# Performance work log

Measured on AMD Instinct MI355X. Metric: run time of the kernel, lower is better.

The kernel has to match this reference:

```python
import jax, jax.numpy as jnp
import numpy as np

E = 8      # number of experts (sublayers)
N = 8192   # tokens / batch rows
D = 1024   # sublayer input size (max_sublayer_input_size)
H = 2048   # sublayer output size
O = 1024   # output_encoding_size


def setup_inputs() -> dict:
    key = jax.random.key(0)
    k0, k1, k2, k3 = jax.random.split(key, 4)
    x_feat = jax.random.normal(k0, (N, D), dtype=jnp.float32)
    expert_idx = jax.random.randint(k1, (N,), 0, E)  # exclusive (top-1) routing
    # Stacked expert params: sublayers = Linear(D,H), encoders = Linear(H,O)
    W1 = jax.random.normal(k2, (E, D, H), dtype=jnp.float32) * (1.0 / np.sqrt(D))
    b1 = jnp.zeros((E, H), dtype=jnp.float32)
    W2 = jax.random.normal(k3, (E, H, O), dtype=jnp.float32) * (1.0 / np.sqrt(H))
    b2 = jnp.zeros((E, O), dtype=jnp.float32)
    return {"x_feat": x_feat, "W1": W1, "b1": b1, "W2": W2, "b2": b2,
            "expert_idx": expert_idx}


def reference(x_feat, W1, b1, W2, b2, expert_idx):
    # one-hot sublayer_mask (last E columns of the original x)
    onehot = jax.nn.one_hot(expert_idx, E, dtype=x_feat.dtype)  # [N, E]
    # Exclusive dispatch: each token goes through exactly one expert.
    # Structural loop over the fixed E experts; combine via the one-hot mask
    # (equivalent to the original gather -> sublayer -> encoder -> scatter).
    enc = jnp.zeros((x_feat.shape[0], O), dtype=x_feat.dtype)
    for i in range(E):
        h = x_feat @ W1[i] + b1[i]          # [N, H] sublayer
        y = h @ W2[i] + b2[i]               # [N, O] encoder
        enc = enc + onehot[:, i:i + 1] * y  # keep only rows routed to expert i
    # output = [encoded (O cols) | sublayer_mask (E cols)]
    return jnp.concatenate([enc, onehot], axis=1)
```

## Files before the change

### kernel.cpp

```cpp
#include <hip/hip_runtime.h>

#define NTOK 8192
#define DDIM 1024
#define HDIM 2048
#define ODIM 1024
#define NEXP 8
#define OUTW (ODIM + NEXP)
#define MT_MAX 64

typedef __bf16 bf16_t;
typedef bf16_t bf16x8 __attribute__((ext_vector_type(8)));
typedef bf16_t bf16x4 __attribute__((ext_vector_type(4)));
typedef float f32x4 __attribute__((ext_vector_type(4)));

__device__ __forceinline__ void gld_lds16(bf16_t* lds, const bf16_t* g) {
  __builtin_amdgcn_global_load_lds(
      (__attribute__((address_space(1))) void*)g,
      (__attribute__((address_space(3))) void*)lds, 16, 0, 0);
}

__global__ void zero_cnt_kernel(int* cnt) {
  if (threadIdx.x < NEXP) cnt[threadIdx.x] = 0;
}

__global__ void route_kernel(const int* __restrict__ idx, float* __restrict__ out,
                             int* __restrict__ rank, int* cnt) {
  __shared__ int lcnt[NEXP];
  __shared__ int lbase[NEXP];
  int t = threadIdx.x;
  if (t < NEXP) lcnt[t] = 0;
  __syncthreads();
  int n = blockIdx.x * 256 + t;
  int e = idx[n];
  int lr = atomicAdd(&lcnt[e], 1);
  __syncthreads();
  if (t < NEXP) lbase[t] = atomicAdd(&cnt[t], lcnt[t]);
  __syncthreads();
  rank[n] = lbase[e] + lr;
  float* o = out + (size_t)n * OUTW + ODIM;
#pragma unroll
  for (int j = 0; j < NEXP; j++) o[j] = (j == e) ? 1.0f : 0.0f;
}

__global__ void scan_kernel(const int* __restrict__ cnt, int* __restrict__ off) {
  if (threadIdx.x == 0) {
    int s = 0;
    for (int e = 0; e < NEXP; e++) { off[e] = s; s += cnt[e]; }
  }
}

__global__ void gather_kernel(const float* __restrict__ x, const int* __restrict__ idx,
                              const int* __restrict__ rank, const int* __restrict__ off,
                              bf16_t* __restrict__ xg, int* __restrict__ tok_of_pos) {
  int n = blockIdx.x;
  int e = idx[n];
  int pos = off[e] + rank[n];
  if (threadIdx.x == 0) tok_of_pos[pos] = n;
  float4 v = ((const float4*)(x + (size_t)n * DDIM))[threadIdx.x];
  bf16x4 o;
  o[0] = (bf16_t)v.x; o[1] = (bf16_t)v.y; o[2] = (bf16_t)v.z; o[3] = (bf16_t)v.w;
  *(bf16x4*)(xg + (size_t)pos * DDIM + threadIdx.x * 4) = o;
}

__global__ __launch_bounds__(256) void wtrans_kernel(const float* __restrict__ src,
                                                     bf16_t* __restrict__ dst,
                                                     int R, int C) {
  __shared__ float t[128][65];
  int e = blockIdx.z;
  int c0 = blockIdx.x * 64, r0g = blockIdx.y * 128;
  int tid = threadIdx.x;
  const float* s = src + (size_t)e * R * C;
#pragma unroll
  for (int p = 0; p < 8; p++) {
    int r = (tid >> 4) + p * 16;
    int c4 = (tid & 15) * 4;
    float4 v = *(const float4*)&s[(size_t)(r0g + r) * C + c0 + c4];
    t[r][c4 + 0] = v.x;
    t[r][c4 + 1] = v.y;
    t[r][c4 + 2] = v.z;
    t[r][c4 + 3] = v.w;
  }
  __syncthreads();
  bf16_t* d = dst + (size_t)e * R * C;
  int w = tid >> 6, l = tid & 63;
#pragma unroll
  for (int itc = 0; itc < 2; itc++) {
#pragma unroll
    for (int it2 = 0; it2 < 2; it2++) {
      int c = (l >> 3) + 8 * w + 32 * itc;
      int r0 = (l & 7) * 8 + 64 * it2;
      bf16x8 o;
#pragma unroll
      for (int j = 0; j < 8; j++) o[j] = (bf16_t)t[r0 + j][c];
      *(bf16x8*)&d[(size_t)(c0 + c) * R + r0g + r0] = o;
    }
  }
}

template <int KDIM, int NCOLS, int MTG, bool TO_BF16>
__global__ __launch_bounds__(256) void gemm_kernel(
    const bf16_t* __restrict__ A, const bf16_t* __restrict__ Bt,
    const float* __restrict__ bias,
    const int* __restrict__ cnt, const int* __restrict__ off,
    const int* __restrict__ tok_of_pos,
    bf16_t* __restrict__ outb, float* __restrict__ outf) {
  constexpr int NT = NCOLS / 128;
  const int b = blockIdx.x;
  const int e = b & 7;
  int t = b >> 3;
  const int mtl = t % MTG;
  t /= MTG;
  const int nt = t % NT;
  const int g = t / NT;
  const int mt = g * MTG + mtl;

  const int count = cnt[e];
  if (mt * 128 >= count) return;
  const int base = off[e];

  __shared__ bf16_t lA[128 * 32];
  __shared__ bf16_t lB[128 * 32];

  const int tid = threadIdx.x;
  const int lane = tid & 63;
  const int wave = tid >> 6;
  const int mrow = lane & 15;
  const int q = lane >> 4;
  const int wm = (wave & 1) * 64;
  const int wn = (wave >> 1) * 64;

  const bf16_t* pA[2];
  const bf16_t* pB[2];
#pragma unroll
  for (int s = 0; s < 2; s++) {
    int lrow = wave * 32 + s * 16 + (lane >> 2);
    int kq = (lane & 3) ^ (lrow & 3);
    int gr = base + mt * 128 + lrow;
    if (gr > NTOK - 1) gr = NTOK - 1;
    pA[s] = A + (size_t)gr * KDIM + kq * 8;
    int nrow = nt * 128 + lrow;
    pB[s] = Bt + ((size_t)e * NCOLS + nrow) * KDIM + kq * 8;
  }

  f32x4 acc[4][4] = {};
  const bf16_t* la0 = &lA[(wm + mrow) * 32 + ((q ^ (mrow & 3)) * 8)];
  const bf16_t* lb0 = &lB[(wn + mrow) * 32 + ((q ^ (mrow & 3)) * 8)];

  for (int kk = 0; kk < KDIM; kk += 32) {
#pragma unroll
    for (int s = 0; s < 2; s++) {
      gld_lds16(&lA[(wave * 2 + s) * 512], pA[s] + kk);
      gld_lds16(&lB[(wave * 2 + s) * 512], pB[s] + kk);
    }
    __syncthreads();
    bf16x8 af[4], bfr[4];
#pragma unroll
    for (int i = 0; i < 4; i++) {
      af[i]  = *(const bf16x8*)(la0 + i * 16 * 32);
      bfr[i] = *(const bf16x8*)(lb0 + i * 16 * 32);
    }
#pragma unroll
    for (int i = 0; i < 4; i++)
#pragma unroll
      for (int j = 0; j < 4; j++)
        acc[i][j] = __builtin_amdgcn_mfma_f32_16x16x32_bf16(af[i], bfr[j], acc[i][j], 0, 0, 0);
    __syncthreads();
  }

  const int mlimit = count - mt * 128;
  float bs[4];
#pragma unroll
  for (int j = 0; j < 4; j++)
    bs[j] = bias[(size_t)e * NCOLS + nt * 128 + wn + j * 16 + mrow];

#pragma unroll
  for (int i = 0; i < 4; i++) {
#pragma unroll
    for (int r = 0; r < 4; r++) {
      int ml = wm + i * 16 + q * 4 + r;
      if (ml < mlimit) {
        int prow = base + mt * 128 + ml;
        if constexpr (TO_BF16) {
          bf16_t* orow = outb + (size_t)prow * NCOLS;
#pragma unroll
          for (int j = 0; j < 4; j++)
            orow[nt * 128 + wn + j * 16 + mrow] = (bf16_t)(acc[i][j][r] + bs[j]);
        } else {
          int tok = tok_of_pos[prow];
          float* orow = outf + (size_t)tok * OUTW;
#pragma unroll
          for (int j = 0; j < 4; j++)
            orow[nt * 128 + wn + j * 16 + mrow] = acc[i][j][r] + bs[j];
        }
      }
    }
  }
}

extern "C" void kernel_launch(void* const* d_in, const int* in_sizes, int n_in,
                              void* d_out, int out_size, void* d_ws, size_t ws_size,
                              hipStream_t stream) {
  const float* x  = (const float*)d_in[0];
  const float* W1 = (const float*)d_in[1];
  const float* b1 = (const float*)d_in[2];
  const float* W2 = (const float*)d_in[3];
  const float* b2 = (const float*)d_in[4];
  const int* idx  = (const int*)d_in[5];
  float* out = (float*)d_out;

  char* ws = (char*)d_ws;
  bf16_t* xg  = (bf16_t*)(ws);
  bf16_t* hg  = (bf16_t*)(ws + 16777216);
  bf16_t* Wt1 = (bf16_t*)(ws + 50331648);
  bf16_t* Wt2 = (bf16_t*)(ws + 83886080);
  int* tok    = (int*)(ws + 117440512);
  int* rank   = (int*)(ws + 117473280);
  int* cnt    = (int*)(ws + 117506048);
  int* off    = (int*)(ws + 117506080);

  zero_cnt_kernel<<<1, 64, 0, stream>>>(cnt);
  route_kernel<<<NTOK / 256, 256, 0, stream>>>(idx, out, rank, cnt);
  scan_kernel<<<1, 64, 0, stream>>>(cnt, off);
  gather_kernel<<<NTOK, 256, 0, stream>>>(x, idx, rank, off, xg, tok);
  wtrans_kernel<<<dim3(HDIM / 64, DDIM / 128, NEXP), 256, 0, stream>>>(W1, Wt1, DDIM, HDIM);
  wtrans_kernel<<<dim3(ODIM / 64, HDIM / 128, NEXP), 256, 0, stream>>>(W2, Wt2, HDIM, ODIM);
  gemm_kernel<DDIM, HDIM, 8, true>
      <<<NEXP * MT_MAX * (HDIM / 128), 256, 0, stream>>>(
      xg, Wt1, b1, cnt, off, tok, hg, nullptr);
  gemm_kernel<HDIM, ODIM, 4, false>
      <<<NEXP * MT_MAX * (ODIM / 128), 256, 0, stream>>>(
      hg, Wt2, b2, cnt, off, tok, nullptr, out);
}
```

Before: 315.9 us.

## Rewrite grouped GEMM as 256x256 tiles with multi-stage LDS pipeline

The grouped expert GEMM moves from 128x128 tiles with 4 waves and a single-buffered LDS loop to 256x256 tiles with 8 waves and a four-slot LDS ring. Global-to-LDS loads are issued several K-steps ahead and paired with explicit waitcnt and barriers, and the MFMA bursts run at raised priority. The aim is to hide load latency behind compute and raise arithmetic intensity. In exchange it uses much more LDS and registers, wastes more work on padded tail tiles per expert, and produces fewer blocks, so the grid may not fill all CUs as well.

```diff
diff --git a/kernel.cpp b/kernel.cpp
--- a/kernel.cpp
+++ b/kernel.cpp
@@ -6,7 +6,7 @@
 #define ODIM 1024
 #define NEXP 8
 #define OUTW (ODIM + NEXP)
-#define MT_MAX 64
+#define MT2 32
 
 typedef __bf16 bf16_t;
 typedef bf16_t bf16x8 __attribute__((ext_vector_type(8)));
@@ -97,100 +97,148 @@
   }
 }
 
-template <int KDIM, int NCOLS, int MTG, bool TO_BF16>
-__global__ __launch_bounds__(256) void gemm_kernel(
+#define BLK(d, kh, mat) ((((d)*2 + (kh)) * 2 + (mat)) * 8192)
+
+#define STAGE(d, kh, mat, P, koff)                                          \
+  {                                                                         \
+    int kw = (koff) & (KDIM - 1);                                           \
+    gld_lds16(&lds[BLK(d, kh, mat) + wave * 512], P[0] + kw);               \
+    gld_lds16(&lds[BLK(d, kh, mat) + 4096 + wave * 512], P[1] + kw);        \
+  }
+
+#define READ_A(d, kh)                                                       \
+  _Pragma("unroll") for (int mi = 0; mi < 8; mi++)                          \
+      af[mi] = *(const bf16x8*)&lds[BLK(d, kh, 0) + aoff + mi * 512];
+
+#define READ_B(d, kh, nh)                                                   \
+  _Pragma("unroll") for (int nj = 0; nj < 2; nj++)                          \
+      bfr[nj] = *(const bf16x8*)&lds[BLK(d, kh, 1) + boff + ((nh)*2 + nj) * 512];
+
+#define MFMA16(nh)                                                          \
+  _Pragma("unroll") for (int mi = 0; mi < 8; mi++)                          \
+  _Pragma("unroll") for (int nj = 0; nj < 2; nj++)                          \
+      acc[mi][(nh)*2 + nj] = __builtin_amdgcn_mfma_f32_16x16x32_bf16(       \
+          af[mi], bfr[nj], acc[mi][(nh)*2 + nj], 0, 0, 0);
+
+#define SYNC_MFMA(nh)                                                       \
+  __builtin_amdgcn_s_barrier();                                             \
+  asm volatile("s_waitcnt lgkmcnt(0)" ::: "memory");                        \
+  __builtin_amdgcn_sched_barrier(0);                                        \
+  __builtin_amdgcn_s_setprio(1);                                            \
+  MFMA16(nh);                                                               \
+  __builtin_amdgcn_s_setprio(0);
+
+#define ENDP_ODD  asm volatile("s_barrier" ::: "memory");
+#define ENDP_EVEN asm volatile("s_waitcnt vmcnt(8)\n\ts_barrier" ::: "memory");
+
+template <int KDIM, int NCOLS, bool TO_BF16>
+__global__ __launch_bounds__(512, 2) void gemm_kernel(
     const bf16_t* __restrict__ A, const bf16_t* __restrict__ Bt,
     const float* __restrict__ bias,
     const int* __restrict__ cnt, const int* __restrict__ off,
     const int* __restrict__ tok_of_pos,
     bf16_t* __restrict__ outb, float* __restrict__ outf) {
-  constexpr int NT = NCOLS / 128;
+  constexpr int NT = NCOLS / 256;
   const int b = blockIdx.x;
   const int e = b & 7;
-  int t = b >> 3;
-  const int mtl = t % MTG;
-  t /= MTG;
+  const int t = b >> 3;
   const int nt = t % NT;
-  const int g = t / NT;
-  const int mt = g * MTG + mtl;
+  const int mt = t / NT;
 
   const int count = cnt[e];
-  if (mt * 128 >= count) return;
+  if (mt * 256 >= count) return;
   const int base = off[e];
 
-  __shared__ bf16_t lA[128 * 32];
-  __shared__ bf16_t lB[128 * 32];
+  __shared__ bf16_t lds[8 * 8192];
 
   const int tid = threadIdx.x;
   const int lane = tid & 63;
   const int wave = tid >> 6;
   const int mrow = lane & 15;
   const int q = lane >> 4;
-  const int wm = (wave & 1) * 64;
-  const int wn = (wave >> 1) * 64;
-
+  const int wrow = (wave >> 2) * 128;
+  const int wcol = (wave & 3) * 64;
+
+  const int rs0 = tid >> 2;
+  const int lch = (tid & 3) ^ (rs0 & 3);
   const bf16_t* pA[2];
   const bf16_t* pB[2];
 #pragma unroll
   for (int s = 0; s < 2; s++) {
-    int lrow = wave * 32 + s * 16 + (lane >> 2);
-    int kq = (lane & 3) ^ (lrow & 3);
-    int gr = base + mt * 128 + lrow;
+    int rs = rs0 + s * 128;
+    int gr = base + mt * 256 + rs;
     if (gr > NTOK - 1) gr = NTOK - 1;
-    pA[s] = A + (size_t)gr * KDIM + kq * 8;
-    int nrow = nt * 128 + lrow;
-    pB[s] = Bt + ((size_t)e * NCOLS + nrow) * KDIM + kq * 8;
-  }
-
-  f32x4 acc[4][4] = {};
-  const bf16_t* la0 = &lA[(wm + mrow) * 32 + ((q ^ (mrow & 3)) * 8)];
-  const bf16_t* lb0 = &lB[(wn + mrow) * 32 + ((q ^ (mrow & 3)) * 8)];
-
-  for (int kk = 0; kk < KDIM; kk += 32) {
-#pragma unroll
-    for (int s = 0; s < 2; s++) {
-      gld_lds16(&lA[(wave * 2 + s) * 512], pA[s] + kk);
-      gld_lds16(&lB[(wave * 2 + s) * 512], pB[s] + kk);
-    }
-    __syncthreads();
-    bf16x8 af[4], bfr[4];
-#pragma unroll
-    for (int i = 0; i < 4; i++) {
-      af[i]  = *(const bf16x8*)(la0 + i * 16 * 32);
-      bfr[i] = *(const bf16x8*)(lb0 + i * 16 * 32);
-    }
-#pragma unroll
-    for (int i = 0; i < 4; i++)
-#pragma unroll
-      for (int j = 0; j < 4; j++)
-        acc[i][j] = __builtin_amdgcn_mfma_f32_16x16x32_bf16(af[i], bfr[j], acc[i][j], 0, 0, 0);
-    __syncthreads();
-  }
-
-  const int mlimit = count - mt * 128;
+    pA[s] = A + (size_t)gr * KDIM + lch * 8;
+    pB[s] = Bt + ((size_t)e * NCOLS + nt * 256 + rs) * KDIM + lch * 8;
+  }
+
+  const int swz = (q ^ (mrow & 3)) * 8;
+  const int aoff = (wrow + mrow) * 32 + swz;
+  const int boff = (wcol + mrow) * 32 + swz;
+
+  f32x4 acc[8][4] = {};
+  bf16x8 af[8], bfr[2];
+
   float bs[4];
 #pragma unroll
   for (int j = 0; j < 4; j++)
-    bs[j] = bias[(size_t)e * NCOLS + nt * 128 + wn + j * 16 + mrow];
-
-#pragma unroll
-  for (int i = 0; i < 4; i++) {
+    bs[j] = bias[(size_t)e * NCOLS + nt * 256 + wcol + j * 16 + mrow];
+
+  STAGE(0, 0, 0, pA, 0);  STAGE(0, 0, 1, pB, 0);
+  STAGE(0, 1, 0, pA, 32); STAGE(0, 1, 1, pB, 32);
+  STAGE(1, 0, 0, pA, 64); STAGE(1, 0, 1, pB, 64);
+  ENDP_EVEN;
+
+  const int NIT = KDIM / 128;
+#pragma unroll 1
+  for (int it = 0; it < NIT; ++it) {
+    const int k0 = it * 128;
+    READ_A(0, 0); READ_B(0, 0, 0);
+    STAGE(1, 1, 0, pA, k0 + 96);
+    SYNC_MFMA(0); ENDP_ODD;
+    READ_B(0, 0, 1);
+    STAGE(1, 1, 1, pB, k0 + 96);
+    SYNC_MFMA(1); ENDP_EVEN;
+    READ_A(0, 1); READ_B(0, 1, 0);
+    STAGE(0, 0, 0, pA, k0 + 128);
+    SYNC_MFMA(0); ENDP_ODD;
+    READ_B(0, 1, 1);
+    STAGE(0, 0, 1, pB, k0 + 128);
+    SYNC_MFMA(1); ENDP_EVEN;
+    READ_A(1, 0); READ_B(1, 0, 0);
+    STAGE(0, 1, 0, pA, k0 + 160);
+    SYNC_MFMA(0); ENDP_ODD;
+    READ_B(1, 0, 1);
+    STAGE(0, 1, 1, pB, k0 + 160);
+    SYNC_MFMA(1); ENDP_EVEN;
+    READ_A(1, 1); READ_B(1, 1, 0);
+    STAGE(1, 0, 0, pA, k0 + 192);
+    SYNC_MFMA(0); ENDP_ODD;
+    READ_B(1, 1, 1);
+    STAGE(1, 0, 1, pB, k0 + 192);
+    SYNC_MFMA(1); ENDP_EVEN;
+  }
+  asm volatile("s_waitcnt vmcnt(0)" ::: "memory");
+
+  const int mlimit = count - mt * 256;
+#pragma unroll
+  for (int mi = 0; mi < 8; mi++) {
 #pragma unroll
     for (int r = 0; r < 4; r++) {
-      int ml = wm + i * 16 + q * 4 + r;
+      int ml = wrow + mi * 16 + q * 4 + r;
       if (ml < mlimit) {
-        int prow = base + mt * 128 + ml;
+        int prow = base + mt * 256 + ml;
         if constexpr (TO_BF16) {
-          bf16_t* orow = outb + (size_t)prow * NCOLS;
+          bf16_t* orow = outb + (size_t)prow * NCOLS + nt * 256;
 #pragma unroll
           for (int j = 0; j < 4; j++)
-            orow[nt * 128 + wn + j * 16 + mrow] = (bf16_t)(acc[i][j][r] + bs[j]);
+            orow[wcol + j * 16 + mrow] = (bf16_t)(acc[mi][j][r] + bs[j]);
         } else {
           int tok = tok_of_pos[prow];
-          float* orow = outf + (size_t)tok * OUTW;
+          float* orow = outf + (size_t)tok * OUTW + nt * 256;
 #pragma unroll
           for (int j = 0; j < 4; j++)
-            orow[nt * 128 + wn + j * 16 + mrow] = acc[i][j][r] + bs[j];
+            orow[wcol + j * 16 + mrow] = acc[mi][j][r] + bs[j];
         }
       }
     }
@@ -224,10 +272,10 @@
   gather_kernel<<<NTOK, 256, 0, stream>>>(x, idx, rank, off, xg, tok);
   wtrans_kernel<<<dim3(HDIM / 64, DDIM / 128, NEXP), 256, 0, stream>>>(W1, Wt1, DDIM, HDIM);
   wtrans_kernel<<<dim3(ODIM / 64, HDIM / 128, NEXP), 256, 0, stream>>>(W2, Wt2, HDIM, ODIM);
-  gemm_kernel<DDIM, HDIM, 8, true>
-      <<<NEXP * MT_MAX * (HDIM / 128), 256, 0, stream>>>(
+  gemm_kernel<DDIM, HDIM, true>
+      <<<NEXP * MT2 * (HDIM / 256), 512, 0, stream>>>(
       xg, Wt1, b1, cnt, off, tok, hg, nullptr);
-  gemm_kernel<HDIM, ODIM, 4, false>
-      <<<NEXP * MT_MAX * (ODIM / 128), 256, 0, stream>>>(
+  gemm_kernel<HDIM, ODIM, false>
+      <<<NEXP * MT2 * (ODIM / 256), 512, 0, stream>>>(
       hg, Wt2, b2, cnt, off, tok, nullptr, out);
 }
```

Measured after the change: 333.7 us. 5.6% more time.

## Double-buffer GEMM LDS tiles and merge the two weight-transpose launches

Applied to the files above, without the earlier changes.

The GEMM main loop now uses two LDS buffers per operand. The global-to-LDS load for the next k-slice is issued before the MFMAs on the current slice, and there is one barrier per iteration instead of two, so load latency is meant to overlap with compute. LDS use per block doubles to 32 KB, which may reduce occupancy. Separately, the two weight transpose/convert launches are merged into a single kernel with a flattened grid, saving one launch and letting the two transposes overlap.

```diff
diff --git a/kernel.cpp b/kernel.cpp
--- a/kernel.cpp
+++ b/kernel.cpp
@@ -62,12 +62,21 @@
   *(bf16x4*)(xg + (size_t)pos * DDIM + threadIdx.x * 4) = o;
 }
 
-__global__ __launch_bounds__(256) void wtrans_kernel(const float* __restrict__ src,
-                                                     bf16_t* __restrict__ dst,
-                                                     int R, int C) {
+__global__ __launch_bounds__(256) void wtrans2_kernel(
+    const float* __restrict__ s1, bf16_t* __restrict__ d1,
+    const float* __restrict__ s2, bf16_t* __restrict__ d2) {
   __shared__ float t[128][65];
-  int e = blockIdx.z;
-  int c0 = blockIdx.x * 64, r0g = blockIdx.y * 128;
+  int b = blockIdx.x;
+  const float* src; bf16_t* dst; int R, C, bx, by, e;
+  if (b < 2048) {
+    src = s1; dst = d1; R = DDIM; C = HDIM;
+    bx = b & 31; by = (b >> 5) & 7; e = b >> 8;
+  } else {
+    int b2 = b - 2048;
+    src = s2; dst = d2; R = HDIM; C = ODIM;
+    bx = b2 & 15; by = (b2 >> 4) & 15; e = b2 >> 8;
+  }
+  int c0 = bx * 64, r0g = by * 128;
   int tid = threadIdx.x;
   const float* s = src + (size_t)e * R * C;
 #pragma unroll
@@ -118,8 +127,8 @@
   if (mt * 128 >= count) return;
   const int base = off[e];
 
-  __shared__ bf16_t lA[128 * 32];
-  __shared__ bf16_t lB[128 * 32];
+  __shared__ bf16_t lA[2][128 * 32];
+  __shared__ bf16_t lB[2][128 * 32];
 
   const int tid = threadIdx.x;
   const int lane = tid & 63;
@@ -143,21 +152,30 @@
   }
 
   f32x4 acc[4][4] = {};
-  const bf16_t* la0 = &lA[(wm + mrow) * 32 + ((q ^ (mrow & 3)) * 8)];
-  const bf16_t* lb0 = &lB[(wn + mrow) * 32 + ((q ^ (mrow & 3)) * 8)];
-
+  const bf16_t* la0 = &lA[0][(wm + mrow) * 32 + ((q ^ (mrow & 3)) * 8)];
+  const bf16_t* lb0 = &lB[0][(wn + mrow) * 32 + ((q ^ (mrow & 3)) * 8)];
+
+#pragma unroll
+  for (int s = 0; s < 2; s++) {
+    gld_lds16(&lA[0][(wave * 2 + s) * 512], pA[s]);
+    gld_lds16(&lB[0][(wave * 2 + s) * 512], pB[s]);
+  }
+  __syncthreads();
+
+  int db = 0;
   for (int kk = 0; kk < KDIM; kk += 32) {
-#pragma unroll
-    for (int s = 0; s < 2; s++) {
-      gld_lds16(&lA[(wave * 2 + s) * 512], pA[s] + kk);
-      gld_lds16(&lB[(wave * 2 + s) * 512], pB[s] + kk);
-    }
-    __syncthreads();
+    if (kk + 32 < KDIM) {
+#pragma unroll
+      for (int s = 0; s < 2; s++) {
+        gld_lds16(&lA[db ^ 1][(wave * 2 + s) * 512], pA[s] + kk + 32);
+        gld_lds16(&lB[db ^ 1][(wave * 2 + s) * 512], pB[s] + kk + 32);
+      }
+    }
     bf16x8 af[4], bfr[4];
 #pragma unroll
     for (int i = 0; i < 4; i++) {
-      af[i]  = *(const bf16x8*)(la0 + i * 16 * 32);
-      bfr[i] = *(const bf16x8*)(lb0 + i * 16 * 32);
+      af[i]  = *(const bf16x8*)(la0 + db * 4096 + i * 16 * 32);
+      bfr[i] = *(const bf16x8*)(lb0 + db * 4096 + i * 16 * 32);
     }
 #pragma unroll
     for (int i = 0; i < 4; i++)
@@ -165,6 +183,7 @@
       for (int j = 0; j < 4; j++)
         acc[i][j] = __builtin_amdgcn_mfma_f32_16x16x32_bf16(af[i], bfr[j], acc[i][j], 0, 0, 0);
     __syncthreads();
+    db ^= 1;
   }
 
   const int mlimit = count - mt * 128;
@@ -222,8 +241,7 @@
   route_kernel<<<NTOK / 256, 256, 0, stream>>>(idx, out, rank, cnt);
   scan_kernel<<<1, 64, 0, stream>>>(cnt, off);
   gather_kernel<<<NTOK, 256, 0, stream>>>(x, idx, rank, off, xg, tok);
-  wtrans_kernel<<<dim3(HDIM / 64, DDIM / 128, NEXP), 256, 0, stream>>>(W1, Wt1, DDIM, HDIM);
-  wtrans_kernel<<<dim3(ODIM / 64, HDIM / 128, NEXP), 256, 0, stream>>>(W2, Wt2, HDIM, ODIM);
+  wtrans2_kernel<<<4096, 256, 0, stream>>>(W1, Wt1, W2, Wt2);
   gemm_kernel<DDIM, HDIM, 8, true>
       <<<NEXP * MT_MAX * (HDIM / 128), 256, 0, stream>>>(
       xg, Wt1, b1, cnt, off, tok, hg, nullptr);
```

New measurement: 326.6 us. 1.03x slower.
